# Optimization experiments

Measured on AMD Instinct MI355X. Metric: run time of the kernel, lower is better.

Reference implementation:

```python
import jax, jax.numpy as jnp
import numpy as np


def _safe_div(w, n):
    # tf.math.divide_no_nan: returns 0 where denominator is 0
    n = n[:, None]
    return jnp.where(n > 0, w / jnp.where(n > 0, n, 1.0), 0.0)


def setup_inputs() -> dict:
    key = jax.random.key(0)
    x = jax.random.normal(key, (16, 32768, 256), dtype=jnp.float32)
    return {"x": x}


def reference(x):
    # x: [n_models, n_samples, dim]
    n_models = x.shape[0]
    xt = jnp.transpose(x, (1, 0, 2))  # [ns, nm, dim]
    v0 = xt[:, 0, :]
    basis_list = [_safe_div(v0, jnp.linalg.norm(v0, axis=1))]  # each [ns, dim]
    for i in range(1, n_models):
        B = jnp.stack(basis_list, axis=1)              # [ns, i, dim]
        v = xt[:, i, :]                                # [ns, dim]
        coef = jnp.einsum('nd,nid->ni', v, B)          # projections onto basis
        w = v - jnp.einsum('ni,nid->nd', coef, B)      # classical Gram-Schmidt step
        basis_list.append(_safe_div(w, jnp.linalg.norm(w, axis=1)))
    return jnp.stack(basis_list, axis=0)               # [n_models, ns, dim]
```

## Files before the change

### kernel.cpp

```cpp
#include <hip/hip_runtime.h>


constexpr int NM = 16;
constexpr int NR = 32768;
constexpr int D4 = 64;

template <int CTRL, int RMASK>
__device__ __forceinline__ float dpp_add(float x) {
    int xi = __builtin_bit_cast(int, x);
    int yi = __builtin_amdgcn_update_dpp(0, xi, CTRL, RMASK, 0xF, false);
    return x + __builtin_bit_cast(float, yi);
}

__device__ __forceinline__ float wave_sum64(float x) {
    x = dpp_add<0xB1,  0xF>(x);
    x = dpp_add<0x4E,  0xF>(x);
    x = dpp_add<0x141, 0xF>(x);
    x = dpp_add<0x140, 0xF>(x);
    x = dpp_add<0x142, 0xA>(x);
    x = dpp_add<0x143, 0xC>(x);
    int s = __builtin_amdgcn_readlane(__builtin_bit_cast(int, x), 63);
    return __builtin_bit_cast(float, s);
}

__device__ __forceinline__ float dot4(const float4& a, const float4& b) {
    return a.x * b.x + a.y * b.y + a.z * b.z + a.w * b.w;
}

__global__ __launch_bounds__(256) void gs_kernel(const float* __restrict__ x,
                                                 float* __restrict__ out) {
    const int lane = threadIdx.x & 63;
    const int wid  = threadIdx.x >> 6;
    const int row  = blockIdx.x * 4 + wid;

    const float4* __restrict__ xi = reinterpret_cast<const float4*>(x);
    float4* __restrict__ oo       = reinterpret_cast<float4*>(out);

    float4 v[NM];
#pragma unroll
    for (int i = 0; i < NM; ++i) {
        v[i] = xi[(size_t)(i * NR + row) * D4 + lane];
    }

    {
        float s   = wave_sum64(dot4(v[0], v[0]));
        float inv = (s > 0.0f) ? rsqrtf(s) : 0.0f;
        v[0].x *= inv; v[0].y *= inv; v[0].z *= inv; v[0].w *= inv;
        oo[(size_t)(0 * NR + row) * D4 + lane] = v[0];
    }

#pragma unroll
    for (int i = 1; i < NM; ++i) {
        float coef[NM - 1];
#pragma unroll
        for (int k = 0; k < i; ++k) {
            coef[k] = wave_sum64(dot4(v[i], v[k]));
        }
#pragma unroll
        for (int k = 0; k < i; ++k) {
            v[i].x -= coef[k] * v[k].x;
            v[i].y -= coef[k] * v[k].y;
            v[i].z -= coef[k] * v[k].z;
            v[i].w -= coef[k] * v[k].w;
        }
        float s   = wave_sum64(dot4(v[i], v[i]));
        float inv = (s > 0.0f) ? rsqrtf(s) : 0.0f;
        v[i].x *= inv; v[i].y *= inv; v[i].z *= inv; v[i].w *= inv;
        oo[(size_t)(i * NR + row) * D4 + lane] = v[i];
    }
}

extern "C" void kernel_launch(void* const* d_in, const int* in_sizes, int n_in,
                              void* d_out, int out_size, void* d_ws, size_t ws_size,
                              hipStream_t stream) {
    const float* x = (const float*)d_in[0];
    float* out     = (float*)d_out;
    dim3 grid(NR / 4);
    dim3 block(256);
    hipLaunchKernelGGL(gs_kernel, grid, block, 0, stream, x, out);
}
```

Baseline: 222.7 us.

## Block Gram-Schmidt into groups of four and launch one wave per row

Restructures classical Gram-Schmidt into blocks of four vectors. Each new block is projected against all previous basis vectors together, and the vectors inside the block are then orthogonalized among themselves. This exposes independent wave reductions across the four vectors of a block, which is meant to hide DPP reduction latency, and it also changes the launch from 256-thread blocks to 64-thread blocks with one row each. The blocked form is a different numerical ordering (block CGS) and stays mathematically equivalent to the reference in exact arithmetic; it may slightly change rounding.

```diff
diff --git a/kernel.cpp b/kernel.cpp
--- a/kernel.cpp
+++ b/kernel.cpp
@@ -27,11 +27,14 @@
     return a.x * b.x + a.y * b.y + a.z * b.z + a.w * b.w;
 }
 
-__global__ __launch_bounds__(256) void gs_kernel(const float* __restrict__ x,
-                                                 float* __restrict__ out) {
-    const int lane = threadIdx.x & 63;
-    const int wid  = threadIdx.x >> 6;
-    const int row  = blockIdx.x * 4 + wid;
+__device__ __forceinline__ void axpy_sub(float4& y, float a, const float4& x) {
+    y.x -= a * x.x; y.y -= a * x.y; y.z -= a * x.z; y.w -= a * x.w;
+}
+
+__global__ __launch_bounds__(64) void gs_kernel(const float* __restrict__ x,
+                                                float* __restrict__ out) {
+    const int lane = threadIdx.x;
+    const int row  = blockIdx.x;
 
     const float4* __restrict__ xi = reinterpret_cast<const float4*>(x);
     float4* __restrict__ oo       = reinterpret_cast<float4*>(out);
@@ -42,31 +45,47 @@
         v[i] = xi[(size_t)(i * NR + row) * D4 + lane];
     }
 
-    {
-        float s   = wave_sum64(dot4(v[0], v[0]));
-        float inv = (s > 0.0f) ? rsqrtf(s) : 0.0f;
-        v[0].x *= inv; v[0].y *= inv; v[0].z *= inv; v[0].w *= inv;
-        oo[(size_t)(0 * NR + row) * D4 + lane] = v[0];
+    auto finalize = [&](int i) {
+        float s   = wave_sum64(dot4(v[i], v[i]));
+        float inv = rsqrtf(s);
+        inv = (s > 0.0f) ? inv : 0.0f;
+        v[i].x *= inv; v[i].y *= inv; v[i].z *= inv; v[i].w *= inv;
+        oo[(size_t)(i * NR + row) * D4 + lane] = v[i];
+    };
+
+    finalize(0);
+#pragma unroll
+    for (int i = 1; i < 4; ++i) {
+        float c[3];
+#pragma unroll
+        for (int k = 0; k < i; ++k) c[k] = wave_sum64(dot4(v[i], v[k]));
+#pragma unroll
+        for (int k = 0; k < i; ++k) axpy_sub(v[i], c[k], v[k]);
+        finalize(i);
     }
 
 #pragma unroll
-    for (int i = 1; i < NM; ++i) {
-        float coef[NM - 1];
+    for (int b = 1; b < 4; ++b) {
+        const int i0 = 4 * b;
 #pragma unroll
-        for (int k = 0; k < i; ++k) {
-            coef[k] = wave_sum64(dot4(v[i], v[k]));
+        for (int ii = 0; ii < 4; ++ii) {
+            float c[12];
+#pragma unroll
+            for (int k = 0; k < i0; ++k) c[k] = wave_sum64(dot4(v[i0 + ii], v[k]));
+#pragma unroll
+            for (int k = 0; k < i0; ++k) axpy_sub(v[i0 + ii], c[k], v[k]);
         }
+        finalize(i0);
 #pragma unroll
-        for (int k = 0; k < i; ++k) {
-            v[i].x -= coef[k] * v[k].x;
-            v[i].y -= coef[k] * v[k].y;
-            v[i].z -= coef[k] * v[k].z;
-            v[i].w -= coef[k] * v[k].w;
+        for (int ii = 1; ii < 4; ++ii) {
+            float c[3];
+#pragma unroll
+            for (int k = 0; k < ii; ++k)
+                c[k] = wave_sum64(dot4(v[i0 + ii], v[i0 + k]));
+#pragma unroll
+            for (int k = 0; k < ii; ++k) axpy_sub(v[i0 + ii], c[k], v[i0 + k]);
+            finalize(i0 + ii);
         }
-        float s   = wave_sum64(dot4(v[i], v[i]));
-        float inv = (s > 0.0f) ? rsqrtf(s) : 0.0f;
-        v[i].x *= inv; v[i].y *= inv; v[i].z *= inv; v[i].w *= inv;
-        oo[(size_t)(i * NR + row) * D4 + lane] = v[i];
     }
 }
 
@@ -75,7 +94,7 @@
                               hipStream_t stream) {
     const float* x = (const float*)d_in[0];
     float* out     = (float*)d_out;
-    dim3 grid(NR / 4);
-    dim3 block(256);
+    dim3 grid(NR);
+    dim3 block(64);
     hipLaunchKernelGGL(gs_kernel, grid, block, 0, stream, x, out);
 }
```

New measurement: 219.4 us. Within noise of the previous version (-1.5%).

## Compute residual norm via Pythagoras to overlap reductions, use one-wave blocks

Applied to the files above, without the earlier changes.

Gets the squared norm of each projected vector from ||v||^2 minus the sum of squared coefficients, so that reduction can be issued together with the coefficient reductions instead of after the subtraction. This shortens the serial chain of wave reductions per step. The projection accumulation is split into two FMA chains to add instruction-level parallelism, and the launch becomes one 64-thread block per row instead of four waves per block. The norm identity only holds if the earlier basis vectors are exactly orthonormal, so it can lose precision through cancellation when a vector is nearly in their span.

```diff
diff --git a/kernel.cpp b/kernel.cpp
--- a/kernel.cpp
+++ b/kernel.cpp
@@ -24,14 +24,13 @@
 }
 
 __device__ __forceinline__ float dot4(const float4& a, const float4& b) {
-    return a.x * b.x + a.y * b.y + a.z * b.z + a.w * b.w;
+    return (a.x * b.x + a.y * b.y) + (a.z * b.z + a.w * b.w);
 }
 
-__global__ __launch_bounds__(256) void gs_kernel(const float* __restrict__ x,
-                                                 float* __restrict__ out) {
-    const int lane = threadIdx.x & 63;
-    const int wid  = threadIdx.x >> 6;
-    const int row  = blockIdx.x * 4 + wid;
+__global__ __launch_bounds__(64) void gs_kernel(const float* __restrict__ x,
+                                                float* __restrict__ out) {
+    const int lane = threadIdx.x;
+    const int row  = blockIdx.x;
 
     const float4* __restrict__ xi = reinterpret_cast<const float4*>(x);
     float4* __restrict__ oo       = reinterpret_cast<float4*>(out);
@@ -51,21 +50,42 @@
 
 #pragma unroll
     for (int i = 1; i < NM; ++i) {
-        float coef[NM - 1];
+        float nn = wave_sum64(dot4(v[i], v[i]));
+        float c[NM - 1];
 #pragma unroll
         for (int k = 0; k < i; ++k) {
-            coef[k] = wave_sum64(dot4(v[i], v[k]));
+            c[k] = wave_sum64(dot4(v[i], v[k]));
+        }
+
+        float s2a = 0.0f, s2b = 0.0f;
+#pragma unroll
+        for (int k = 0; k < i; k += 2) s2a = fmaf(c[k], c[k], s2a);
+#pragma unroll
+        for (int k = 1; k < i; k += 2) s2b = fmaf(c[k], c[k], s2b);
+        float s   = nn - (s2a + s2b);
+        float inv = (s > 0.0f) ? rsqrtf(s) : 0.0f;
+
+        float4 a0 = make_float4(0.f, 0.f, 0.f, 0.f);
+        float4 a1 = make_float4(0.f, 0.f, 0.f, 0.f);
+#pragma unroll
+        for (int k = 0; k < i; k += 2) {
+            a0.x = fmaf(c[k], v[k].x, a0.x);
+            a0.y = fmaf(c[k], v[k].y, a0.y);
+            a0.z = fmaf(c[k], v[k].z, a0.z);
+            a0.w = fmaf(c[k], v[k].w, a0.w);
         }
 #pragma unroll
-        for (int k = 0; k < i; ++k) {
-            v[i].x -= coef[k] * v[k].x;
-            v[i].y -= coef[k] * v[k].y;
-            v[i].z -= coef[k] * v[k].z;
-            v[i].w -= coef[k] * v[k].w;
+        for (int k = 1; k < i; k += 2) {
+            a1.x = fmaf(c[k], v[k].x, a1.x);
+            a1.y = fmaf(c[k], v[k].y, a1.y);
+            a1.z = fmaf(c[k], v[k].z, a1.z);
+            a1.w = fmaf(c[k], v[k].w, a1.w);
         }
-        float s   = wave_sum64(dot4(v[i], v[i]));
-        float inv = (s > 0.0f) ? rsqrtf(s) : 0.0f;
-        v[i].x *= inv; v[i].y *= inv; v[i].z *= inv; v[i].w *= inv;
+
+        v[i].x = (v[i].x - (a0.x + a1.x)) * inv;
+        v[i].y = (v[i].y - (a0.y + a1.y)) * inv;
+        v[i].z = (v[i].z - (a0.z + a1.z)) * inv;
+        v[i].w = (v[i].w - (a0.w + a1.w)) * inv;
         oo[(size_t)(i * NR + row) * D4 + lane] = v[i];
     }
 }
@@ -75,7 +95,7 @@
                               hipStream_t stream) {
     const float* x = (const float*)d_in[0];
     float* out     = (float*)d_out;
-    dim3 grid(NR / 4);
-    dim3 block(256);
+    dim3 grid(NR);
+    dim3 block(64);
     hipLaunchKernelGGL(gs_kernel, grid, block, 0, stream, x, out);
 }
```

Result: faster. 207.7 us (-6.8%).
